# Kernel optimization log

Measured on AMD Instinct MI355X. Metric: run time of the kernel, lower is better.

The kernel has to match this reference:

```python
import jax, jax.numpy as jnp
import numpy as np

TEMP = 0.05
MOMENTUM = 0.2
SMOOTH = 0.1
TAU_W = 0.09
NUM_SAMPLES = 100000
NUM_FEATURES = 256
BATCH = 256


def _l2norm(x, axis=1, eps=1e-12):
    return x / jnp.maximum(jnp.linalg.norm(x, axis=axis, keepdims=True), eps)


def setup_inputs() -> dict:
    key = jax.random.key(0)
    k1, k2, k3, k4 = jax.random.split(key, 4)
    inputs1 = jax.random.normal(k1, (BATCH, NUM_FEATURES), dtype=jnp.float32)
    inputs2 = jax.random.normal(k2, (BATCH, NUM_FEATURES), dtype=jnp.float32)
    features = jax.random.normal(k3, (NUM_SAMPLES, NUM_FEATURES), dtype=jnp.float32)
    features = _l2norm(features)  # memory bank holds unit-norm centroids
    targets = jax.random.randint(k4, (BATCH,), 0, NUM_SAMPLES)
    return {"inputs1": inputs1, "inputs2": inputs2, "features": features, "targets": targets}


def reference(inputs1, inputs2, features, targets):
    # ---- ClusterMemory.forward (mode='wgm') ----
    x1 = _l2norm(inputs1)                      # F.normalize(inputs1)
    x2 = _l2norm(inputs2)                      # F.normalize(inputs2)
    outputs = (x1 @ features.T) / TEMP         # [B, N] logits vs memory bank
    regression = (x2 @ features.T) / TEMP      # [B, N]

    logp = jax.nn.log_softmax(outputs, axis=1)
    # CrossEntropyLoss
    loss_c = -jnp.mean(jnp.take_along_axis(logp, targets[:, None], axis=1))
    # SoftEntropySmooth: smoothed mix of soft targets (detached) and one-hot
    onehot = jax.nn.one_hot(targets, features.shape[0], dtype=logp.dtype)
    smooth_t = jax.lax.stop_gradient(
        (1.0 - SMOOTH) * jax.nn.softmax(regression, axis=1) + SMOOTH * onehot
    )
    loss_s = jnp.sum(jnp.mean(-smooth_t * logp, axis=0))

    # ---- CM_WgtMean memory update: per-cluster segment softmax + scatter ----
    N = features.shape[0]
    d = jnp.sum(x1 * features[targets], axis=1)            # [B] sim to own centroid
    logits = -d / TAU_W
    segmax = jax.ops.segment_max(logits, targets, num_segments=N)   # [N]
    e = jnp.exp(logits - segmax[targets])                  # stable per-segment exp
    denom = jax.ops.segment_sum(e, targets, num_segments=N)
    w = e / denom[targets]                                 # segment softmax weights
    wmean = jax.ops.segment_sum(w[:, None] * x1, targets, num_segments=N)  # [N, D]
    counts = jax.ops.segment_sum(jnp.ones_like(d), targets, num_segments=N)
    upd = _l2norm(MOMENTUM * features + (1.0 - MOMENTUM) * wmean)
    new_features = jnp.where((counts > 0)[:, None], upd, features)

    return loss_c, loss_s, new_features
```

## Files before the change

kernel.cpp:

```cpp
#include <hip/hip_runtime.h>
#include <stdint.h>
#include <stddef.h>

#define TEMP      0.05f
#define INV_TEMP  20.0f
#define MOMENTUM  0.2f
#define SMOOTH    0.1f
#define TAU_W     0.09f
#define NSAMP     100000
#define NFEAT     256
#define BATCH     256
#define SHIFT     20.0f
#define MT        64
#define TILES     1563
#define NSHADOW   16

typedef float  f32x4  __attribute__((ext_vector_type(4)));
typedef float  f32x2  __attribute__((ext_vector_type(2)));
typedef short  short8 __attribute__((ext_vector_type(8)));
typedef unsigned int u32x2 __attribute__((ext_vector_type(2)));

__device__ __forceinline__ short f2bf(float f) {
    uint32_t u = __builtin_bit_cast(uint32_t, f);
    u = (u + 0x7fffu + ((u >> 16) & 1u)) >> 16;
    return (short)u;
}

__device__ __forceinline__ void mfma_bf16(f32x4& c, short8 a, short8 b) {
    asm("v_mfma_f32_16x16x32_bf16 %0, %1, %2, %0" : "+v"(c) : "v"(a), "v"(b));
}

__device__ __forceinline__ void gload_lds16(const short* g, short* l) {
    __builtin_amdgcn_global_load_lds(
        (const __attribute__((address_space(1))) unsigned int*)(const void*)g,
        (__attribute__((address_space(3))) unsigned int*)(void*)l,
        16, 0, 0);
}

__device__ __forceinline__ float block_reduce_sum256(float v, float* scratch) {
    for (int o = 32; o > 0; o >>= 1) v += __shfl_down(v, o, 64);
    int lane = threadIdx.x & 63, wid = threadIdx.x >> 6;
    if (lane == 0) scratch[wid] = v;
    __syncthreads();
    if (threadIdx.x == 0)
        scratch[4] = scratch[0] + scratch[1] + scratch[2] + scratch[3];
    __syncthreads();
    return scratch[4];
}

__global__ void __launch_bounds__(256)
k_conv(const float* __restrict__ F, short* __restrict__ Fb, float* outCopy) {
    int t = threadIdx.x;
    int row = blockIdx.x * 4 + (t >> 6);
    int c4  = t & 63;
    f32x4 v = {0.f, 0.f, 0.f, 0.f};
    bool live = row < NSAMP;
    if (live) v = *(const f32x4*)(F + (size_t)row * NFEAT + c4 * 4);
    if (outCopy != nullptr && live) {
        float* op = outCopy + 2 + (size_t)row * NFEAT + c4 * 4;
        __builtin_nontemporal_store(f32x2{v[0], v[1]}, (f32x2*)op);
        __builtin_nontemporal_store(f32x2{v[2], v[3]}, (f32x2*)(op + 2));
    }
    int tile = row >> 6, mf = (row >> 4) & 3, l15 = row & 15;
    int kk = c4 >> 3, lg = (c4 >> 1) & 3, half = c4 & 1;
    uint32_t p0 = (uint32_t)(uint16_t)f2bf(v[0]) | ((uint32_t)(uint16_t)f2bf(v[1]) << 16);
    uint32_t p1 = (uint32_t)(uint16_t)f2bf(v[2]) | ((uint32_t)(uint16_t)f2bf(v[3]) << 16);
    size_t off = (size_t)tile * 16384 + (size_t)(((kk * 4 + mf) * 64 + lg * 16 + l15) * 8) + half * 4;
    *(u32x2*)(Fb + off) = (u32x2){p0, p1};
}

__global__ void __launch_bounds__(256)
k_copy(const float* __restrict__ F, float* __restrict__ out) {
    const size_t total = (size_t)NSAMP * NFEAT / 4;
    size_t stride = (size_t)gridDim.x * 256;
    for (size_t i = (size_t)blockIdx.x * 256 + threadIdx.x; i < total; i += stride) {
        f32x4 v = *(const f32x4*)(F + i * 4);
        float* op = out + 2 + i * 4;
        __builtin_nontemporal_store(f32x2{v[0], v[1]}, (f32x2*)op);
        __builtin_nontemporal_store(f32x2{v[2], v[3]}, (f32x2*)(op + 2));
    }
}

__global__ void k_prep(const float* __restrict__ in1, const float* __restrict__ in2,
                       const float* __restrict__ F, const int* __restrict__ tgt,
                       float* __restrict__ x1n, short* __restrict__ XbF,
                       float* __restrict__ dvec, float* __restrict__ Zs) {
    __shared__ float scratch[8];
    int b = blockIdx.x;
    int k = threadIdx.x;
    int gid = b * NFEAT + k;
    if (gid < NSHADOW * BATCH * 3) Zs[gid] = 0.f;
    float v1 = in1[b * NFEAT + k];
    float v2 = in2[b * NFEAT + k];
    float n1 = block_reduce_sum256(v1 * v1, scratch);
    float n2 = block_reduce_sum256(v2 * v2, scratch);
    float x1 = v1 / fmaxf(sqrtf(n1), 1e-12f);
    float x2 = v2 / fmaxf(sqrtf(n2), 1e-12f);
    x1n[b * NFEAT + k] = x1;
    int w = b >> 5, r = b & 31;
    int cf = r >> 4, l15 = r & 15;
    int kk = k >> 5, lg = (k >> 3) & 3, j = k & 7;
    int lane = lg * 16 + l15;
    XbF[(((w * 4 + cf) * 8 + kk) * 64 + lane) * 8 + j]     = f2bf(x1);
    XbF[(((w * 4 + 2 + cf) * 8 + kk) * 64 + lane) * 8 + j] = f2bf(x2);
    int t = tgt[b];
    float dv = block_reduce_sum256(x1 * F[(size_t)t * NFEAT + k], scratch);
    if (k == 0) dvec[b] = dv;
}

__global__ void __launch_bounds__(512, 4)
k_main(const short* __restrict__ Fb, const short* __restrict__ XbF,
       float* __restrict__ Zs) {
    __shared__ short lfs[16384];
    int tid = threadIdx.x, w = tid >> 6, lane = tid & 63;
    size_t tbase = (size_t)blockIdx.x * 16384;

    #pragma unroll
    for (int j = 0; j < 4; ++j)
        gload_lds16(Fb + tbase + (size_t)((w * 4 + j) * 512 + lane * 8),
                    &lfs[(w * 4 + j) * 512]);
    __syncthreads();

    int l15 = lane & 15, lg = lane >> 4;
    int m0 = blockIdx.x * MT;
    f32x4 acc[4][4] = {};
    const short* xw = XbF + (size_t)w * 16384 + lane * 8;

    #pragma unroll
    for (int kk = 0; kk < 8; ++kk) {
        short8 bf0 = *(const short8*)(xw + (0 * 8 + kk) * 512);
        short8 bf1 = *(const short8*)(xw + (1 * 8 + kk) * 512);
        short8 bf2 = *(const short8*)(xw + (2 * 8 + kk) * 512);
        short8 bf3 = *(const short8*)(xw + (3 * 8 + kk) * 512);
        short8 a0 = *(const short8*)(&lfs[(kk * 4 + 0) * 512 + lane * 8]);
        short8 a1 = *(const short8*)(&lfs[(kk * 4 + 1) * 512 + lane * 8]);
        short8 a2 = *(const short8*)(&lfs[(kk * 4 + 2) * 512 + lane * 8]);
        short8 a3 = *(const short8*)(&lfs[(kk * 4 + 3) * 512 + lane * 8]);
        mfma_bf16(acc[0][0], a0, bf0); mfma_bf16(acc[0][1], a0, bf1);
        mfma_bf16(acc[0][2], a0, bf2); mfma_bf16(acc[0][3], a0, bf3);
        mfma_bf16(acc[1][0], a1, bf0); mfma_bf16(acc[1][1], a1, bf1);
        mfma_bf16(acc[1][2], a1, bf2); mfma_bf16(acc[1][3], a1, bf3);
        mfma_bf16(acc[2][0], a2, bf0); mfma_bf16(acc[2][1], a2, bf1);
        mfma_bf16(acc[2][2], a2, bf2); mfma_bf16(acc[2][3], a2, bf3);
        mfma_bf16(acc[3][0], a3, bf0); mfma_bf16(acc[3][1], a3, bf1);
        mfma_bf16(acc[3][2], a3, bf2); mfma_bf16(acc[3][3], a3, bf3);
    }

    int sh = (blockIdx.x & (NSHADOW - 1)) * BATCH;
    #pragma unroll
    for (int cf = 0; cf < 2; ++cf) {
        float z1 = 0.f, z2 = 0.f, s12 = 0.f;
        #pragma unroll
        for (int mf = 0; mf < 4; ++mf) {
            #pragma unroll
            for (int q = 0; q < 4; ++q) {
                int grow = m0 + mf * 16 + lg * 4 + q;
                if (grow < NSAMP) {
                    float l1 = acc[mf][cf][q] * INV_TEMP;
                    float e1 = __expf(l1 - SHIFT);
                    float e2 = __expf(acc[mf][cf + 2][q] * INV_TEMP - SHIFT);
                    z1 += e1; z2 += e2; s12 += e2 * l1;
                }
            }
        }
        z1  += __shfl_xor(z1, 16);  z1  += __shfl_xor(z1, 32);
        z2  += __shfl_xor(z2, 16);  z2  += __shfl_xor(z2, 32);
        s12 += __shfl_xor(s12, 16); s12 += __shfl_xor(s12, 32);
        if (lane < 16) {
            int b = w * 32 + cf * 16 + lane;
            atomicAdd(&Zs[sh + b], z1);
            atomicAdd(&Zs[NSHADOW * BATCH + sh + b], z2);
            atomicAdd(&Zs[2 * NSHADOW * BATCH + sh + b], s12);
        }
    }
}

__global__ void k_tail(const float* __restrict__ F, const int* __restrict__ tgt,
                       const float* __restrict__ dvec, const float* __restrict__ x1n,
                       const float* __restrict__ Zs, float* __restrict__ out) {
    __shared__ float scratch[8];
    if (blockIdx.x == BATCH) {
        int b = threadIdx.x;
        float z1 = 0.f, z2 = 0.f, s12 = 0.f;
        #pragma unroll
        for (int j = 0; j < NSHADOW; ++j) {
            z1  += Zs[j * BATCH + b];
            z2  += Zs[NSHADOW * BATCH + j * BATCH + b];
            s12 += Zs[2 * NSHADOW * BATCH + j * BATCH + b];
        }
        float L1   = SHIFT + logf(z1);
        float lpt  = dvec[b] * INV_TEMP - L1;
        float ce12 = s12 / z2;
        float lc = -lpt;
        float ls = (1.f - SMOOTH) * (L1 - ce12) + SMOOTH * (-lpt);
        float sc = block_reduce_sum256(lc, scratch);
        float ss = block_reduce_sum256(ls, scratch);
        if (b == 0) {
            out[0] = sc / (float)BATCH;
            out[1] = ss / (float)BATCH;
        }
        return;
    }
    __shared__ int   stgt[BATCH];
    __shared__ float slog[BATCH];
    int b = blockIdx.x, k = threadIdx.x;
    stgt[k] = tgt[k];
    slog[k] = -dvec[k] * (1.0f / TAU_W);
    __syncthreads();
    int t = stgt[b];
    for (int bp = 0; bp < b; ++bp)
        if (stgt[bp] == t) return;
    float m = -1e30f;
    for (int bp = 0; bp < BATCH; ++bp)
        if (stgt[bp] == t) m = fmaxf(m, slog[bp]);
    float denom = 0.f;
    for (int bp = 0; bp < BATCH; ++bp)
        if (stgt[bp] == t) denom += expf(slog[bp] - m);
    float wmean = 0.f;
    for (int bp = 0; bp < BATCH; ++bp)
        if (stgt[bp] == t)
            wmean += expf(slog[bp] - m) * x1n[bp * NFEAT + k];
    wmean /= denom;
    float upd = MOMENTUM * F[(size_t)t * NFEAT + k] + (1.f - MOMENTUM) * wmean;
    float nrm = block_reduce_sum256(upd * upd, scratch);
    out[2 + (size_t)t * NFEAT + k] = upd / fmaxf(sqrtf(nrm), 1e-12f);
}

extern "C" void kernel_launch(void* const* d_in, const int* in_sizes, int n_in,
                              void* d_out, int out_size, void* d_ws, size_t ws_size,
                              hipStream_t stream) {
    const float* in1 = (const float*)d_in[0];
    const float* in2 = (const float*)d_in[1];
    const float* F   = (const float*)d_in[2];
    const int*   tgt = (const int*)d_in[3];
    float* out = (float*)d_out;

    char* ws = (char*)d_ws;
    float* x1n = (float*)ws;
    short* XbF = (short*)(ws + 262144);
    float* dv  = (float*)(ws + 524288);
    float* Zs  = (float*)(ws + 525312);
    const size_t FB_BYTES = (size_t)TILES * 32768;
    const size_t NEED     = 589824 + FB_BYTES;

    if (ws_size >= NEED) {
        short* Fb = (short*)(ws + 589824);
        hipLaunchKernelGGL(k_conv, dim3(TILES * 16), dim3(256), 0, stream, F, Fb, out);
        hipLaunchKernelGGL(k_prep, dim3(BATCH), dim3(256), 0, stream,
                           in1, in2, F, tgt, x1n, XbF, dv, Zs);
        hipLaunchKernelGGL(k_main, dim3(TILES), dim3(512), 0, stream, Fb, XbF, Zs);
        hipLaunchKernelGGL(k_tail, dim3(BATCH + 1), dim3(256), 0, stream,
                           F, tgt, dv, x1n, Zs, out);
    } else {
        short* Fb = (short*)((char*)d_out + 51183616);
        hipLaunchKernelGGL(k_conv, dim3(TILES * 16), dim3(256), 0, stream, F, Fb, (float*)nullptr);
        hipLaunchKernelGGL(k_prep, dim3(BATCH), dim3(256), 0, stream,
                           in1, in2, F, tgt, x1n, XbF, dv, Zs);
        hipLaunchKernelGGL(k_main, dim3(TILES), dim3(512), 0, stream, Fb, XbF, Zs);
        hipLaunchKernelGGL(k_copy, dim3(2048), dim3(256), 0, stream, F, out);
        hipLaunchKernelGGL(k_tail, dim3(BATCH + 1), dim3(256), 0, stream,
                           F, tgt, dv, x1n, Zs, out);
    }
}
```

Measured before the change: 299.0 us.

## Fuse prep and bf16 conversion into one front kernel with aligned copy stores

```diff
diff --git a/kernel.cpp b/kernel.cpp
--- a/kernel.cpp
+++ b/kernel.cpp
@@ -14,11 +14,13 @@
 #define MT        64
 #define TILES     1563
 #define NSHADOW   16
+#define PREPB     256
+#define COPYB     2048
 
 typedef float  f32x4  __attribute__((ext_vector_type(4)));
 typedef float  f32x2  __attribute__((ext_vector_type(2)));
 typedef short  short8 __attribute__((ext_vector_type(8)));
-typedef unsigned int u32x2 __attribute__((ext_vector_type(2)));
+typedef unsigned int u32x4 __attribute__((ext_vector_type(4)));
 
 __device__ __forceinline__ short f2bf(float f) {
     uint32_t u = __builtin_bit_cast(uint32_t, f);
@@ -49,63 +51,90 @@
 }
 
 __global__ void __launch_bounds__(256)
-k_conv(const float* __restrict__ F, short* __restrict__ Fb, float* outCopy) {
-    int t = threadIdx.x;
-    int row = blockIdx.x * 4 + (t >> 6);
-    int c4  = t & 63;
-    f32x4 v = {0.f, 0.f, 0.f, 0.f};
-    bool live = row < NSAMP;
-    if (live) v = *(const f32x4*)(F + (size_t)row * NFEAT + c4 * 4);
-    if (outCopy != nullptr && live) {
-        float* op = outCopy + 2 + (size_t)row * NFEAT + c4 * 4;
-        __builtin_nontemporal_store(f32x2{v[0], v[1]}, (f32x2*)op);
-        __builtin_nontemporal_store(f32x2{v[2], v[3]}, (f32x2*)(op + 2));
-    }
-    int tile = row >> 6, mf = (row >> 4) & 3, l15 = row & 15;
-    int kk = c4 >> 3, lg = (c4 >> 1) & 3, half = c4 & 1;
-    uint32_t p0 = (uint32_t)(uint16_t)f2bf(v[0]) | ((uint32_t)(uint16_t)f2bf(v[1]) << 16);
-    uint32_t p1 = (uint32_t)(uint16_t)f2bf(v[2]) | ((uint32_t)(uint16_t)f2bf(v[3]) << 16);
-    size_t off = (size_t)tile * 16384 + (size_t)(((kk * 4 + mf) * 64 + lg * 16 + l15) * 8) + half * 4;
-    *(u32x2*)(Fb + off) = (u32x2){p0, p1};
+k_front(const float* __restrict__ in1, const float* __restrict__ in2,
+        const float* __restrict__ F, const int* __restrict__ tgt,
+        float* __restrict__ x1n, short* __restrict__ XbF,
+        float* __restrict__ dvec, float* __restrict__ Zs,
+        short* __restrict__ Fb, float* outCopy) {
+    int tid = threadIdx.x;
+    if (blockIdx.x < PREPB) {
+        __shared__ float scratch[8];
+        int b = blockIdx.x;
+        int k = tid;
+        int gid = b * NFEAT + k;
+        if (gid < NSHADOW * BATCH * 3) Zs[gid] = 0.f;
+        float v1 = in1[b * NFEAT + k];
+        float v2 = in2[b * NFEAT + k];
+        float n1 = block_reduce_sum256(v1 * v1, scratch);
+        float n2 = block_reduce_sum256(v2 * v2, scratch);
+        float x1 = v1 / fmaxf(sqrtf(n1), 1e-12f);
+        float x2 = v2 / fmaxf(sqrtf(n2), 1e-12f);
+        x1n[b * NFEAT + k] = x1;
+        int w = b >> 5, r = b & 31;
+        int cf = r >> 4, l15 = r & 15;
+        int kk = k >> 5, lg = (k >> 3) & 3, j = k & 7;
+        int lane = lg * 16 + l15;
+        XbF[(((w * 4 + cf) * 8 + kk) * 64 + lane) * 8 + j]     = f2bf(x1);
+        XbF[(((w * 4 + 2 + cf) * 8 + kk) * 64 + lane) * 8 + j] = f2bf(x2);
+        int t = tgt[b];
+        float dv = block_reduce_sum256(x1 * F[(size_t)t * NFEAT + k], scratch);
+        if (k == 0) dvec[b] = dv;
+        return;
+    }
+    size_t gid    = (size_t)(blockIdx.x - PREPB) * 256 + tid;
+    size_t stride = (size_t)COPYB * 256;
+    const size_t total16 = (size_t)NSAMP * NFEAT / 4;
+
+    if (outCopy != nullptr) {
+        for (size_t j = gid + 1; j < total16; j += stride) {
+            f32x2 lo = *(const f32x2*)(F + 4 * j - 2);
+            f32x2 hi = *(const f32x2*)(F + 4 * j);
+            __builtin_nontemporal_store(f32x4{lo[0], lo[1], hi[0], hi[1]},
+                                        (f32x4*)(outCopy + 4 * j));
+        }
+        if (gid == 0) {
+            outCopy[2] = F[0];
+            outCopy[3] = F[1];
+            outCopy[total16 * 4]     = F[total16 * 4 - 2];
+            outCopy[total16 * 4 + 1] = F[total16 * 4 - 1];
+        }
+    }
+    const size_t totalB = (size_t)TILES * MT * 32;
+    for (size_t u = gid; u < totalB; u += stride) {
+        int row = (int)(u >> 5), c8 = (int)(u & 31);
+        f32x4 v0 = {0.f, 0.f, 0.f, 0.f}, v1 = {0.f, 0.f, 0.f, 0.f};
+        if (row < NSAMP) {
+            v0 = *(const f32x4*)(F + (size_t)row * NFEAT + c8 * 8);
+            v1 = *(const f32x4*)(F + (size_t)row * NFEAT + c8 * 8 + 4);
+        }
+        int tile = row >> 6, mf = (row >> 4) & 3, l15 = row & 15;
+        int kk = c8 >> 2, lg = c8 & 3;
+        uint32_t p0 = (uint32_t)(uint16_t)f2bf(v0[0]) | ((uint32_t)(uint16_t)f2bf(v0[1]) << 16);
+        uint32_t p1 = (uint32_t)(uint16_t)f2bf(v0[2]) | ((uint32_t)(uint16_t)f2bf(v0[3]) << 16);
+        uint32_t p2 = (uint32_t)(uint16_t)f2bf(v1[0]) | ((uint32_t)(uint16_t)f2bf(v1[1]) << 16);
+        uint32_t p3 = (uint32_t)(uint16_t)f2bf(v1[2]) | ((uint32_t)(uint16_t)f2bf(v1[3]) << 16);
+        size_t off = (size_t)tile * 16384 + (size_t)(((kk * 4 + mf) * 64 + lg * 16 + l15) * 8);
+        *(u32x4*)(Fb + off) = (u32x4){p0, p1, p2, p3};
+    }
 }
 
 __global__ void __launch_bounds__(256)
 k_copy(const float* __restrict__ F, float* __restrict__ out) {
-    const size_t total = (size_t)NSAMP * NFEAT / 4;
+    const size_t total16 = (size_t)NSAMP * NFEAT / 4;
     size_t stride = (size_t)gridDim.x * 256;
-    for (size_t i = (size_t)blockIdx.x * 256 + threadIdx.x; i < total; i += stride) {
-        f32x4 v = *(const f32x4*)(F + i * 4);
-        float* op = out + 2 + i * 4;
-        __builtin_nontemporal_store(f32x2{v[0], v[1]}, (f32x2*)op);
-        __builtin_nontemporal_store(f32x2{v[2], v[3]}, (f32x2*)(op + 2));
-    }
-}
-
-__global__ void k_prep(const float* __restrict__ in1, const float* __restrict__ in2,
-                       const float* __restrict__ F, const int* __restrict__ tgt,
-                       float* __restrict__ x1n, short* __restrict__ XbF,
-                       float* __restrict__ dvec, float* __restrict__ Zs) {
-    __shared__ float scratch[8];
-    int b = blockIdx.x;
-    int k = threadIdx.x;
-    int gid = b * NFEAT + k;
-    if (gid < NSHADOW * BATCH * 3) Zs[gid] = 0.f;
-    float v1 = in1[b * NFEAT + k];
-    float v2 = in2[b * NFEAT + k];
-    float n1 = block_reduce_sum256(v1 * v1, scratch);
-    float n2 = block_reduce_sum256(v2 * v2, scratch);
-    float x1 = v1 / fmaxf(sqrtf(n1), 1e-12f);
-    float x2 = v2 / fmaxf(sqrtf(n2), 1e-12f);
-    x1n[b * NFEAT + k] = x1;
-    int w = b >> 5, r = b & 31;
-    int cf = r >> 4, l15 = r & 15;
-    int kk = k >> 5, lg = (k >> 3) & 3, j = k & 7;
-    int lane = lg * 16 + l15;
-    XbF[(((w * 4 + cf) * 8 + kk) * 64 + lane) * 8 + j]     = f2bf(x1);
-    XbF[(((w * 4 + 2 + cf) * 8 + kk) * 64 + lane) * 8 + j] = f2bf(x2);
-    int t = tgt[b];
-    float dv = block_reduce_sum256(x1 * F[(size_t)t * NFEAT + k], scratch);
-    if (k == 0) dvec[b] = dv;
+    size_t gid = (size_t)blockIdx.x * 256 + threadIdx.x;
+    for (size_t j = gid + 1; j < total16; j += stride) {
+        f32x2 lo = *(const f32x2*)(F + 4 * j - 2);
+        f32x2 hi = *(const f32x2*)(F + 4 * j);
+        __builtin_nontemporal_store(f32x4{lo[0], lo[1], hi[0], hi[1]},
+                                    (f32x4*)(out + 4 * j));
+    }
+    if (gid == 0) {
+        out[2] = F[0];
+        out[3] = F[1];
+        out[total16 * 4]     = F[total16 * 4 - 2];
+        out[total16 * 4 + 1] = F[total16 * 4 - 1];
+    }
 }
 
 __global__ void __launch_bounds__(512, 4)
@@ -245,17 +274,15 @@
 
     if (ws_size >= NEED) {
         short* Fb = (short*)(ws + 589824);
-        hipLaunchKernelGGL(k_conv, dim3(TILES * 16), dim3(256), 0, stream, F, Fb, out);
-        hipLaunchKernelGGL(k_prep, dim3(BATCH), dim3(256), 0, stream,
-                           in1, in2, F, tgt, x1n, XbF, dv, Zs);
+        hipLaunchKernelGGL(k_front, dim3(PREPB + COPYB), dim3(256), 0, stream,
+                           in1, in2, F, tgt, x1n, XbF, dv, Zs, Fb, out);
         hipLaunchKernelGGL(k_main, dim3(TILES), dim3(512), 0, stream, Fb, XbF, Zs);
         hipLaunchKernelGGL(k_tail, dim3(BATCH + 1), dim3(256), 0, stream,
                            F, tgt, dv, x1n, Zs, out);
     } else {
         short* Fb = (short*)((char*)d_out + 51183616);
-        hipLaunchKernelGGL(k_conv, dim3(TILES * 16), dim3(256), 0, stream, F, Fb, (float*)nullptr);
-        hipLaunchKernelGGL(k_prep, dim3(BATCH), dim3(256), 0, stream,
-                           in1, in2, F, tgt, x1n, XbF, dv, Zs);
+        hipLaunchKernelGGL(k_front, dim3(PREPB + COPYB), dim3(256), 0, stream,
+                           in1, in2, F, tgt, x1n, XbF, dv, Zs, Fb, (float*)nullptr);
         hipLaunchKernelGGL(k_main, dim3(TILES), dim3(512), 0, stream, Fb, XbF, Zs);
         hipLaunchKernelGGL(k_copy, dim3(2048), dim3(256), 0, stream, F, out);
         hipLaunchKernelGGL(k_tail, dim3(BATCH + 1), dim3(256), 0, stream,
```

Result: slower. 310.5 us (+3.8%).
